# Performance work log

Measured on AMD Instinct MI355X. Metric: run time of the kernel, lower is better.

The kernel has to match this reference:

```python
import jax, jax.numpy as jnp
import numpy as np

D_MODEL = 2048
D_INNER = 4096
D_CONV = 4
D_STATE = 16
DT_RANK = 128  # (d_model + 15) // 16
EPS = 1e-5
B_SZ, SEQ = 2, 2048


def _silu(x):
    return x * jax.nn.sigmoid(x)


def setup_inputs() -> dict:
    key = jax.random.key(0)
    ks = jax.random.split(key, 10)
    s = lambda k, shape, sc=0.02: jax.random.normal(k, shape, jnp.float32) * sc
    # S4D-real init for A_log, small negative bias for dt (standard Mamba init)
    A_log = jnp.log(jnp.tile(jnp.arange(1, D_STATE + 1, dtype=jnp.float32), (D_INNER, 1)))
    return {
        "hidden_states": jax.random.normal(ks[0], (B_SZ, SEQ, D_MODEL), jnp.float32),
        "norm_scale": jnp.ones((D_MODEL,), jnp.float32),
        "in_proj_w": s(ks[1], (2 * D_INNER, D_MODEL)),
        "conv_w": s(ks[2], (D_INNER, 1, D_CONV), 0.1),
        "conv_b": s(ks[3], (D_INNER,), 0.1),
        "x_proj_w": s(ks[4], (DT_RANK + 2 * D_STATE, D_INNER)),
        "dt_proj_w": s(ks[5], (D_INNER, DT_RANK), 0.1),
        "dt_proj_b": jnp.full((D_INNER,), -4.0, jnp.float32) + s(ks[6], (D_INNER,), 0.1),
        "out_proj_w": s(ks[7], (D_MODEL, D_INNER)),
        "A_log": A_log,
        "D": jnp.ones((D_INNER,), jnp.float32),
    }


def reference(hidden_states, norm_scale, in_proj_w, conv_w, conv_b, x_proj_w,
              dt_proj_w, dt_proj_b, out_proj_w, A_log, D):
    B, L, _ = hidden_states.shape
    residual = hidden_states
    # RMSNorm
    rms = jnp.sqrt(jnp.mean(hidden_states ** 2, axis=-1, keepdims=True) + EPS)
    xn = hidden_states / rms * norm_scale
    # in_proj -> [B, L, 2*d_inner]; torch code keeps this as projected_states
    xz = jnp.einsum('bld,ed->ble', xn, in_proj_w)
    x_in = xz[..., :D_INNER].transpose(0, 2, 1)  # [B, d_inner, L]
    z = xz[..., D_INNER:]                        # [B, L, d_inner]
    # depthwise causal conv1d (padding d_conv-1, truncated to L) + SiLU
    xc = jax.lax.conv_general_dilated(
        x_in, conv_w, window_strides=(1,), padding=[(D_CONV - 1, 0)],
        feature_group_count=D_INNER)
    xc = _silu(xc + conv_b[None, :, None])       # [B, d_inner, L]
    # x_proj -> dt, B, C
    x_dbl = jnp.einsum('bdl,rd->brl', xc, x_proj_w)  # [B, dt_rank+2*d_state, L]
    dt_low = x_dbl[:, :DT_RANK]
    Bm = x_dbl[:, DT_RANK:DT_RANK + D_STATE]         # [B, d_state, L]
    Cm = x_dbl[:, DT_RANK + D_STATE:]                # [B, d_state, L]
    delta = jax.nn.softplus(
        jnp.einsum('dr,brl->bdl', dt_proj_w, dt_low) + dt_proj_b[None, :, None])
    A = -jnp.exp(A_log)                              # [d_inner, d_state]
    # selective scan: h_t = exp(delta_t * A) * h_{t-1} + delta_t * B_t * u_t
    delta_t = delta.transpose(2, 0, 1)  # [L, B, d_inner]
    u_t = xc.transpose(2, 0, 1)         # [L, B, d_inner]
    B_t = Bm.transpose(2, 0, 1)         # [L, B, d_state]
    C_t = Cm.transpose(2, 0, 1)         # [L, B, d_state]

    def step(h, inp):
        d_, b_, c_, u_ = inp
        dA = jnp.exp(d_[..., None] * A)                      # [B, d_inner, d_state]
        h = h * dA + (d_ * u_)[..., None] * b_[:, None, :]   # [B, d_inner, d_state]
        y = jnp.einsum('bds,bs->bd', h, c_)                  # [B, d_inner]
        return h, y

    h0 = jnp.zeros((B, D_INNER, D_STATE), hidden_states.dtype)
    _, ys = jax.lax.scan(step, h0, (delta_t, B_t, C_t, u_t))  # [L, B, d_inner]
    y = ys.transpose(1, 0, 2) + xc.transpose(0, 2, 1) * D     # [B, L, d_inner]
    y = y * _silu(z)
    out = jnp.einsum('bld,od->blo', y, out_proj_w)            # [B, L, d_model]
    return residual + out, xz
```

## Files before the change

kernel.cpp:

```cpp
#include <hip/hip_runtime.h>
#include <cstdint>
#include <cstddef>

#define DM   2048
#define DI   4096
#define DST  16
#define DTR  128
#define SEQL 2048
#define NTOK 4096
#define XZW  8192
#define NCHAIN 8192
#define CL   32
#define NCH  64

typedef short short8 __attribute__((ext_vector_type(8)));
typedef float f32x4 __attribute__((ext_vector_type(4)));

__device__ __forceinline__ short f2bf(float x) {
  union { float f; uint32_t u; } v; v.f = x;
  uint32_t r = v.u + 0x7fffu + ((v.u >> 16) & 1u);
  return (short)(r >> 16);
}
__device__ __forceinline__ float bf2f(short s) {
  union { uint32_t u; float f; } v; v.u = ((uint32_t)(uint16_t)s) << 16;
  return v.f;
}

__device__ __forceinline__ void stage16(const short* g, short* l) {
#if __has_builtin(__builtin_amdgcn_global_load_lds)
  __builtin_amdgcn_global_load_lds((const __attribute__((address_space(1))) void*)g,
                                   (__attribute__((address_space(3))) void*)l, 16, 0, 0);
#else
  *(short8*)l = *(const short8*)g;
#endif
}

__global__ __launch_bounds__(256) void cvt4_k(const float* __restrict__ in,
                                              short* __restrict__ out, int n4) {
  int i = blockIdx.x * 256 + threadIdx.x;
  if (i >= n4) return;
  float4 v = ((const float4*)in)[i];
  short4 o;
  o.x = f2bf(v.x); o.y = f2bf(v.y); o.z = f2bf(v.z); o.w = f2bf(v.w);
  ((short4*)out)[i] = o;
}

__global__ __launch_bounds__(256) void pad_xproj_k(const float* __restrict__ xp,
                                                   short* __restrict__ out) {
  int i = blockIdx.x * 256 + threadIdx.x;
  if (i >= 256 * 1024) return;
  int r = i >> 10;
  float4 v = make_float4(0.f, 0.f, 0.f, 0.f);
  if (r < 160) v = ((const float4*)xp)[i];
  short4 o;
  o.x = f2bf(v.x); o.y = f2bf(v.y); o.z = f2bf(v.z); o.w = f2bf(v.w);
  ((short4*)out)[i] = o;
}

__global__ __launch_bounds__(256) void rmsnorm_k(const float* __restrict__ hs,
                                                 const float* __restrict__ sc,
                                                 short* __restrict__ xn) {
  const int token = blockIdx.x;
  const int tid = threadIdx.x;
  const float* row = hs + (size_t)token * DM;
  float4 a = ((const float4*)row)[tid];
  float4 b = ((const float4*)row)[tid + 256];
  float ss = a.x*a.x + a.y*a.y + a.z*a.z + a.w*a.w
           + b.x*b.x + b.y*b.y + b.z*b.z + b.w*b.w;
  #pragma unroll
  for (int o = 32; o > 0; o >>= 1) ss += __shfl_xor(ss, o);
  __shared__ float wsum[4];
  if ((tid & 63) == 0) wsum[tid >> 6] = ss;
  __syncthreads();
  float tot = wsum[0] + wsum[1] + wsum[2] + wsum[3];
  float inv = rsqrtf(tot * (1.0f / DM) + 1e-5f);
  float4 s1 = ((const float4*)sc)[tid];
  float4 s2 = ((const float4*)sc)[tid + 256];
  short4 o1, o2;
  o1.x = f2bf(a.x * inv * s1.x); o1.y = f2bf(a.y * inv * s1.y);
  o1.z = f2bf(a.z * inv * s1.z); o1.w = f2bf(a.w * inv * s1.w);
  o2.x = f2bf(b.x * inv * s2.x); o2.y = f2bf(b.y * inv * s2.y);
  o2.z = f2bf(b.z * inv * s2.z); o2.w = f2bf(b.w * inv * s2.w);
  ((short4*)xn)[(size_t)token * (DM / 4) + tid] = o1;
  ((short4*)xn)[(size_t)token * (DM / 4) + tid + 256] = o2;
}

#define LGKM_FENCE() do { asm volatile("s_waitcnt lgkmcnt(0)" ::: "memory"); \
                          __builtin_amdgcn_sched_barrier(0); } while (0)

template <int MFR, int EPI, int RBY, int RBX, int PRE>
__global__ __launch_bounds__(512) void gemm_big(const short* __restrict__ A,
                                                const short* __restrict__ B,
                                                int K, int N, int nbx,
                                                float* __restrict__ out_f,
                                                const float* __restrict__ aux_f) {
  constexpr int BM = MFR * 32;
  constexpr int ABYTES = BM * 128;
  constexpr int BBYTES = 256 * 128;
  constexpr int AINSTR = ABYTES / 8192;
  constexpr int BUF = ABYTES + BBYTES;
  __shared__ char lds[2 * BUF];

  const int tid = threadIdx.x;
  const int lane = tid & 63;
  const int wid = tid >> 6;
  const int wm = wid >> 2;
  const int wn = wid & 3;
  const int lr = lane & 15;
  const int lj = lane >> 4;

  const int xcd = blockIdx.x & 7;
  const int idx = blockIdx.x >> 3;
  const int nrgx = nbx / RBX;
  const int by = (xcd / nrgx) * RBY + idx / RBX;
  const int bx = (xcd % nrgx) * RBX + idx % RBX;
  const size_t m0 = (size_t)by * BM;
  const size_t n0 = (size_t)bx * 256;

  const int NT = K >> 6;

  auto stA1 = [&](int t, char* buf, int s) {
    const int k0 = t << 6;
    const int off = s * 8192 + tid * 16;
    const int r = off >> 7;
    const int j = (off >> 4) & 7;
    stage16(A + (m0 + r) * (size_t)K + k0 + ((j ^ (r & 7)) << 3),
            (short*)(buf + off));
  };
  auto stB1 = [&](int t, char* buf, int s) {
    const int k0 = t << 6;
    const int off = s * 8192 + tid * 16;
    const int r = off >> 7;
    const int j = (off >> 4) & 7;
    stage16(B + (n0 + r) * (size_t)K + k0 + ((j ^ (r & 7)) << 3),
            (short*)(buf + ABYTES + off));
  };

#define READ_A(dst, fbase)                                                   \
  _Pragma("unroll")                                                          \
  for (int f = 0; f < MFR / 2; ++f) {                                        \
    const int arow = wm * (BM / 2) + ((fbase) + f) * 16 + lr;                \
    _Pragma("unroll")                                                        \
    for (int ks = 0; ks < 2; ++ks)                                           \
      dst[f][ks] = *(const short8*)(cur + arow * 128 +                       \
                     ((((ks << 2) + lj) ^ (arow & 7)) << 4));                \
  }
#define READ_B(dst, gbase)                                                   \
  _Pragma("unroll")                                                          \
  for (int g = 0; g < 2; ++g) {                                              \
    const int brow = wn * 64 + ((gbase) + g) * 16 + lr;                      \
    _Pragma("unroll")                                                        \
    for (int ks = 0; ks < 2; ++ks)                                           \
      dst[g][ks] = *(const short8*)(cur + ABYTES + brow * 128 +              \
                     ((((ks << 2) + lj) ^ (brow & 7)) << 4));                \
  }
#define MFMA_Q(fbase, gbase, bvx)                                            \
  __builtin_amdgcn_s_setprio(1);                                             \
  _Pragma("unroll")                                                          \
  for (int ks = 0; ks < 2; ++ks)                                             \
    _Pragma("unroll")                                                        \
    for (int f = 0; f < MFR / 2; ++f)                                        \
      _Pragma("unroll")                                                      \
      for (int g = 0; g < 2; ++g)                                            \
        acc[(fbase) + f][(gbase) + g] = __builtin_amdgcn_mfma_f32_16x16x32_bf16( \
            av[f][ks], bvx[g][ks], acc[(fbase) + f][(gbase) + g], 0, 0, 0);  \
  __builtin_amdgcn_s_setprio(0);

  f32x4 acc[MFR][4] = {};

  {
    #pragma unroll
    for (int s = 0; s < AINSTR; ++s) stA1(0, lds, s);
    #pragma unroll
    for (int s = 0; s < 4; ++s) stB1(0, lds, s);
    if (PRE && NT > 1) { stA1(1, lds + BUF, 0); stA1(1, lds + BUF, 2); }
    if (PRE && NT > 1) asm volatile("s_waitcnt vmcnt(2)" ::: "memory");
    else               asm volatile("s_waitcnt vmcnt(0)" ::: "memory");
    __builtin_amdgcn_s_barrier();
    __builtin_amdgcn_sched_barrier(0);
  }

  for (int t = 0; t < NT; ++t) {
    char* cur = lds + (t & 1) * BUF;
    char* nxt = lds + ((t + 1) & 1) * BUF;
    const bool m1 = (t + 1) < NT;
    const bool m2 = (t + 2) < NT;
    short8 av[MFR / 2][2], bv0[2][2], bv1[2][2];

    READ_A(av, 0);
    READ_B(bv0, 0);
    if (m1) {
      if constexpr (PRE) { stA1(t + 1, nxt, 1); stA1(t + 1, nxt, 3); }
      else {
        #pragma unroll
        for (int s = 0; s < AINSTR; ++s) stA1(t + 1, nxt, s);
      }
    }
    LGKM_FENCE();
    MFMA_Q(0, 0, bv0);
    __builtin_amdgcn_s_barrier();

    READ_B(bv1, 2);
    if (m1) { stB1(t + 1, nxt, 0); stB1(t + 1, nxt, 1); }
    LGKM_FENCE();
    MFMA_Q(0, 2, bv1);
    __builtin_amdgcn_s_barrier();

    READ_A(av, MFR / 2);
    if (m1) { stB1(t + 1, nxt, 2); stB1(t + 1, nxt, 3); }
    if (PRE && m2) { stA1(t + 2, cur, 0); stA1(t + 2, cur, 2); }
    LGKM_FENCE();
    MFMA_Q(MFR / 2, 2, bv1);
    __builtin_amdgcn_s_barrier();

    MFMA_Q(MFR / 2, 0, bv0);
    if (PRE && m2) asm volatile("s_waitcnt vmcnt(2)" ::: "memory");
    else           asm volatile("s_waitcnt vmcnt(0)" ::: "memory");
    __builtin_amdgcn_s_barrier();
    __builtin_amdgcn_sched_barrier(0);
  }

  #pragma unroll
  for (int f = 0; f < MFR; ++f)
    #pragma unroll
    for (int g = 0; g < 4; ++g)
      #pragma unroll
      for (int jj = 0; jj < 4; ++jj) {
        const size_t row = m0 + wm * (BM / 2) + f * 16 + lj * 4 + jj;
        const size_t col = n0 + wn * 64 + g * 16 + lr;
        float v = acc[f][g][jj];
        if constexpr (EPI == 3) v += aux_f[row * (size_t)N + col];
        out_f[row * (size_t)N + col] = v;
      }
#undef READ_A
#undef READ_B
#undef MFMA_Q
}

template <int EPI>
__global__ __launch_bounds__(256) void gemm_nt(const short* __restrict__ A,
                                               const short* __restrict__ B,
                                               int ld, int K, int N,
                                               float* __restrict__ out_f,
                                               const float* __restrict__ aux_f,
                                               short* __restrict__ out_bf) {
  __shared__ short As[128 * 64];
  __shared__ short Bs[128 * 64];
  const int tid = threadIdx.x;
  const int lane = tid & 63;
  const int wid = tid >> 6;
  const int wr = wid >> 1, wc = wid & 1;
  const size_t m0 = (size_t)blockIdx.y * 128;
  const size_t n0 = (size_t)blockIdx.x * 128;
  A += (size_t)blockIdx.z * K;
  B += (size_t)blockIdx.z * K;
  f32x4 acc[4][4] = {};
  for (int k0 = 0; k0 < K; k0 += 64) {
    #pragma unroll
    for (int i = 0; i < 4; ++i) {
      const int off = i * 4096 + tid * 16;
      const int r = off >> 7;
      const int ke = (off & 127) >> 1;
      stage16(A + (m0 + r) * (size_t)ld + k0 + ke, &As[off >> 1]);
      stage16(B + (n0 + r) * (size_t)ld + k0 + ke, &Bs[off >> 1]);
    }
    __syncthreads();
    #pragma unroll
    for (int kk = 0; kk < 64; kk += 32) {
      short8 af[4], bfr[4];
      const int kb = kk + (lane >> 4) * 8;
      const int rr = lane & 15;
      #pragma unroll
      for (int f = 0; f < 4; ++f) {
        af[f]  = *(const short8*)&As[(wr * 64 + f * 16 + rr) * 64 + kb];
        bfr[f] = *(const short8*)&Bs[(wc * 64 + f * 16 + rr) * 64 + kb];
      }
      #pragma unroll
      for (int fm = 0; fm < 4; ++fm)
        #pragma unroll
        for (int fn = 0; fn < 4; ++fn)
          acc[fm][fn] = __builtin_amdgcn_mfma_f32_16x16x32_bf16(af[fm], bfr[fn], acc[fm][fn], 0, 0, 0);
    }
    __syncthreads();
  }
  const int rbase = (lane >> 4) * 4;
  const int cbase = lane & 15;
  #pragma unroll
  for (int fm = 0; fm < 4; ++fm) {
    #pragma unroll
    for (int fn = 0; fn < 4; ++fn) {
      #pragma unroll
      for (int j = 0; j < 4; ++j) {
        const size_t row = m0 + wr * 64 + fm * 16 + rbase + j;
        const size_t col = n0 + wc * 64 + fn * 16 + cbase;
        const float v = acc[fm][fn][j];
        if constexpr (EPI == 2) {
          float x = v + aux_f[col];
          float sp = (x > 20.f) ? x : log1pf(__expf(x));
          out_bf[row * (size_t)N + col] = f2bf(sp);
        } else {
          out_f[((size_t)blockIdx.z * NTOK + row) * (size_t)N + col] = v;
        }
      }
    }
  }
}

__global__ __launch_bounds__(256) void xdbl_epi_k(const float* __restrict__ part,
                                                  short* __restrict__ dtl,
                                                  float* __restrict__ Bc,
                                                  float* __restrict__ Cc) {
  const int row = blockIdx.x;
  const int col = threadIdx.x;
  const size_t i = (size_t)row * 256 + col;
  const float v = part[i] + part[(size_t)NTOK * 256 + i]
                + part[(size_t)2 * NTOK * 256 + i]
                + part[(size_t)3 * NTOK * 256 + i];
  if (col < 128)      dtl[(size_t)row * 128 + col] = f2bf(v);
  else if (col < 144) Bc[(size_t)row * 16 + (col - 128)] = v;
  else if (col < 160) Cc[(size_t)row * 16 + (col - 144)] = v;
}

__global__ __launch_bounds__(256) void conv_silu_k(const float* __restrict__ xz,
                                                   const float* __restrict__ cw,
                                                   const float* __restrict__ cb,
                                                   short* __restrict__ xc) {
  const int d = blockIdx.x * 256 + threadIdx.x;
  const int t0 = blockIdx.y * 8;
  const int l0 = t0 & (SEQL - 1);
  const float4 w = ((const float4*)cw)[d];
  const float bias = cb[d];
  float x0 = (l0 >= 3) ? xz[(size_t)(t0 - 3) * XZW + d] : 0.f;
  float x1 = (l0 >= 2) ? xz[(size_t)(t0 - 2) * XZW + d] : 0.f;
  float x2 = (l0 >= 1) ? xz[(size_t)(t0 - 1) * XZW + d] : 0.f;
  #pragma unroll
  for (int i = 0; i < 8; ++i) {
    const float x3 = xz[(size_t)(t0 + i) * XZW + d];
    const float acc = bias + w.x * x0 + w.y * x1 + w.z * x2 + w.w * x3;
    const float sv = acc / (1.f + __expf(-acc));
    xc[(size_t)(t0 + i) * DI + d] = f2bf(sv);
    x0 = x1; x1 = x2; x2 = x3;
  }
}

__global__ __launch_bounds__(256) void scan1_k(const short* __restrict__ del_bf,
                                               const short* __restrict__ xc,
                                               const float* __restrict__ Bc,
                                               const float* __restrict__ alog,
                                               float* __restrict__ hloc,
                                               float* __restrict__ Ssum) {
  const int t = blockIdx.x * 256 + threadIdx.x;
  const int sub = t & 1;
  const int chain = (t >> 1) & (NCHAIN - 1);
  const int chunk = t >> 14;
  const int b = chain >> 12;
  const int d = chain & 4095;
  float A[8];
  #pragma unroll
  for (int j = 0; j < 8; ++j) A[j] = -__expf(alog[d * 16 + sub * 8 + j]);
  float h[8] = {};
  float S = 0.f;
  size_t token = (size_t)b * SEQL + (size_t)chunk * CL;
  #pragma unroll 2
  for (int l = 0; l < CL; ++l, ++token) {
    const float delta = bf2f(del_bf[token * DI + d]);
    const float u = bf2f(xc[token * DI + d]);
    const float du = delta * u;
    S += delta;
    const float4 B0 = ((const float4*)Bc)[token * 4 + sub * 2];
    const float4 B1 = ((const float4*)Bc)[token * 4 + sub * 2 + 1];
    const float Bv[8] = {B0.x, B0.y, B0.z, B0.w, B1.x, B1.y, B1.z, B1.w};
    #pragma unroll
    for (int j = 0; j < 8; ++j)
      h[j] = h[j] * __expf(delta * A[j]) + du * Bv[j];
  }
  const size_t idx = (size_t)(chunk * NCHAIN + chain) * 4 + sub * 2;
  ((float4*)hloc)[idx]     = make_float4(h[0], h[1], h[2], h[3]);
  ((float4*)hloc)[idx + 1] = make_float4(h[4], h[5], h[6], h[7]);
  if (sub == 0) Ssum[chunk * NCHAIN + chain] = S;
}

__global__ __launch_bounds__(256) void scan2_k(float* __restrict__ hloc,
                                               const float* __restrict__ Ssum,
                                               const float* __restrict__ alog) {
  const int t = blockIdx.x * 256 + threadIdx.x;
  const int q = t & 3;
  const int chain = t >> 2;
  const int d = chain & 4095;
  float A[4];
  #pragma unroll
  for (int j = 0; j < 4; ++j) A[j] = -__expf(alog[d * 16 + q * 4 + j]);
  float4 h = make_float4(0.f, 0.f, 0.f, 0.f);
  for (int c = 0; c < NCH; ++c) {
    const size_t idx = (size_t)(c * NCHAIN + chain) * 4 + q;
    const float S = Ssum[c * NCHAIN + chain];
    const float4 hl = ((const float4*)hloc)[idx];
    ((float4*)hloc)[idx] = h;
    h.x = h.x * __expf(A[0] * S) + hl.x;
    h.y = h.y * __expf(A[1] * S) + hl.y;
    h.z = h.z * __expf(A[2] * S) + hl.z;
    h.w = h.w * __expf(A[3] * S) + hl.w;
  }
}

__global__ __launch_bounds__(256) void scan3_k(const short* __restrict__ del_bf,
                                               const short* __restrict__ xc,
                                               const float* __restrict__ Bc,
                                               const float* __restrict__ Cc,
                                               const float* __restrict__ xzbuf,
                                               const float* __restrict__ alog,
                                               const float* __restrict__ dvec,
                                               const float* __restrict__ hin,
                                               short* __restrict__ y) {
  const int t = blockIdx.x * 256 + threadIdx.x;
  const int sub = t & 1;
  const int chain = (t >> 1) & (NCHAIN - 1);
  const int chunk = t >> 14;
  const int b = chain >> 12;
  const int d = chain & 4095;
  float A[8];
  #pragma unroll
  for (int j = 0; j < 8; ++j) A[j] = -__expf(alog[d * 16 + sub * 8 + j]);
  const float Dd = dvec[d];
  const size_t idx = (size_t)(chunk * NCHAIN + chain) * 4 + sub * 2;
  const float4 h0 = ((const float4*)hin)[idx];
  const float4 h1 = ((const float4*)hin)[idx + 1];
  float h[8] = {h0.x, h0.y, h0.z, h0.w, h1.x, h1.y, h1.z, h1.w};
  size_t token = (size_t)b * SEQL + (size_t)chunk * CL;
  #pragma unroll 2
  for (int l = 0; l < CL; ++l, ++token) {
    const float delta = bf2f(del_bf[token * DI + d]);
    const float u = bf2f(xc[token * DI + d]);
    const float du = delta * u;
    const float4 B0 = ((const float4*)Bc)[token * 4 + sub * 2];
    const float4 B1 = ((const float4*)Bc)[token * 4 + sub * 2 + 1];
    const float4 C0 = ((const float4*)Cc)[token * 4 + sub * 2];
    const float4 C1 = ((const float4*)Cc)[token * 4 + sub * 2 + 1];
    const float Bv[8] = {B0.x, B0.y, B0.z, B0.w, B1.x, B1.y, B1.z, B1.w};
    const float Cv[8] = {C0.x, C0.y, C0.z, C0.w, C1.x, C1.y, C1.z, C1.w};
    float yp = 0.f;
    #pragma unroll
    for (int j = 0; j < 8; ++j) {
      h[j] = h[j] * __expf(delta * A[j]) + du * Bv[j];
      yp += h[j] * Cv[j];
    }
    yp += __shfl_xor(yp, 1);
    if (sub == 0) {
      const float z = xzbuf[token * XZW + DI + d];
      const float sz = z / (1.f + __expf(-z));
      y[token * DI + d] = f2bf((yp + u * Dd) * sz);
    }
  }
}

extern "C" void kernel_launch(void* const* d_in, const int* in_sizes, int n_in,
                              void* d_out, int out_size, void* d_ws, size_t ws_size,
                              hipStream_t stream) {
  const float* hs   = (const float*)d_in[0];
  const float* nsc  = (const float*)d_in[1];
  const float* win  = (const float*)d_in[2];
  const float* cw   = (const float*)d_in[3];
  const float* cb   = (const float*)d_in[4];
  const float* wxp  = (const float*)d_in[5];
  const float* wdt  = (const float*)d_in[6];
  const float* bdt  = (const float*)d_in[7];
  const float* wout = (const float*)d_in[8];
  const float* alog = (const float*)d_in[9];
  const float* dvec = (const float*)d_in[10];

  float* out0 = (float*)d_out;
  float* xz   = out0 + (size_t)NTOK * DM;

  char* w = (char*)d_ws;
  size_t off = 0;
  auto alloc = [&](size_t bytes) {
    char* p = w + off;
    off += (bytes + 255) & ~(size_t)255;
    return p;
  };
  short* xn_bf   = (short*)alloc((size_t)NTOK * DM * 2);
  short* win_bf  = (short*)alloc((size_t)XZW * DM * 2);
  short* wout_bf = (short*)alloc((size_t)DM * DI * 2);
  short* wdt_bf  = (short*)alloc((size_t)DI * DTR * 2);
  short* wxp_bf  = (short*)alloc((size_t)256 * DI * 2);
  short* xc_bf   = (short*)alloc((size_t)NTOK * DI * 2);
  short* dtl_bf  = (short*)alloc((size_t)NTOK * DTR * 2);
  float* Bc      = (float*)alloc((size_t)NTOK * DST * 4);
  float* Cc      = (float*)alloc((size_t)NTOK * DST * 4);
  short* del_bf  = (short*)alloc((size_t)NTOK * DI * 2);
  short* y_bf    = (short*)alloc((size_t)NTOK * DI * 2);

  float* xp_part = (float*)win_bf;
  float* hloc    = (float*)win_bf;
  float* Ssum    = (float*)xn_bf;

  cvt4_k<<<16384, 256, 0, stream>>>(win,  win_bf,  (XZW * DM) / 4);
  cvt4_k<<<8192,  256, 0, stream>>>(wout, wout_bf, (DM * DI) / 4);
  cvt4_k<<<512,   256, 0, stream>>>(wdt,  wdt_bf,  (DI * DTR) / 4);
  pad_xproj_k<<<1024, 256, 0, stream>>>(wxp, wxp_bf);

  rmsnorm_k<<<NTOK, 256, 0, stream>>>(hs, nsc, xn_bf);
  gemm_big<8, 0, 8, 8, 1><<<dim3((XZW / 256) * (NTOK / 256)), 512, 0, stream>>>(
      xn_bf, win_bf, DM, XZW, XZW / 256, xz, nullptr);
  conv_silu_k<<<dim3(DI / 256, NTOK / 8), 256, 0, stream>>>(xz, cw, cb, xc_bf);
  gemm_nt<4><<<dim3(2, NTOK / 128, 4), 256, 0, stream>>>(
      xc_bf, wxp_bf, DI, DI / 4, 256, xp_part, nullptr, nullptr);
  xdbl_epi_k<<<NTOK, 256, 0, stream>>>(xp_part, dtl_bf, Bc, Cc);
  gemm_nt<2><<<dim3(DI / 128, NTOK / 128, 1), 256, 0, stream>>>(
      dtl_bf, wdt_bf, DTR, DTR, DI, nullptr, bdt, del_bf);
  scan1_k<<<(NCHAIN * 2 * NCH) / 256, 256, 0, stream>>>(
      del_bf, xc_bf, Bc, alog, hloc, Ssum);
  scan2_k<<<(NCHAIN * 4) / 256, 256, 0, stream>>>(hloc, Ssum, alog);
  scan3_k<<<(NCHAIN * 2 * NCH) / 256, 256, 0, stream>>>(
      del_bf, xc_bf, Bc, Cc, xz, alog, dvec, hloc, y_bf);
  gemm_big<4, 3, 8, 4, 0><<<dim3((DM / 256) * (NTOK / 128)), 512, 0, stream>>>(
      y_bf, wout_bf, DI, DM, DM / 256, out0, hs);
}
```

Baseline: 570.7 us.

## Stage B tiles through registers in big GEMM and skip padded x_proj columns

The big GEMM no longer prefetches A two tiles ahead. B tiles for the next step are now loaded from global memory into registers early in each iteration and written to LDS at the end, replacing the direct global-to-LDS staging of B. This is meant to hide B load latency behind the MFMA work, at the cost of more registers and an extra LDS write phase. Separately, the x_proj GEMM epilogue and the reduction kernel skip the padded columns at or beyond 160, saving wasted stores and reads.

Measured after the change: 573.6 us. Within noise of the previous version (+0.5%).

```diff
diff --git a/kernel.cpp b/kernel.cpp
--- a/kernel.cpp
+++ b/kernel.cpp
@@ -88,7 +88,7 @@
 #define LGKM_FENCE() do { asm volatile("s_waitcnt lgkmcnt(0)" ::: "memory"); \
                           __builtin_amdgcn_sched_barrier(0); } while (0)
 
-template <int MFR, int EPI, int RBY, int RBX, int PRE>
+template <int MFR, int EPI, int RBY, int RBX>
 __global__ __launch_bounds__(512) void gemm_big(const short* __restrict__ A,
                                                 const short* __restrict__ B,
                                                 int K, int N, int nbx,
@@ -135,6 +135,13 @@
     stage16(B + (n0 + r) * (size_t)K + k0 + ((j ^ (r & 7)) << 3),
             (short*)(buf + ABYTES + off));
   };
+  auto bsrc = [&](int t, int s) -> const int4* {
+    const int k0 = t << 6;
+    const int off = s * 8192 + tid * 16;
+    const int r = off >> 7;
+    const int j = (off >> 4) & 7;
+    return (const int4*)(B + (n0 + r) * (size_t)K + k0 + ((j ^ (r & 7)) << 3));
+  };
 
 #define READ_A(dst, fbase)                                                   \
   _Pragma("unroll")                                                          \
@@ -173,9 +180,7 @@
     for (int s = 0; s < AINSTR; ++s) stA1(0, lds, s);
     #pragma unroll
     for (int s = 0; s < 4; ++s) stB1(0, lds, s);
-    if (PRE && NT > 1) { stA1(1, lds + BUF, 0); stA1(1, lds + BUF, 2); }
-    if (PRE && NT > 1) asm volatile("s_waitcnt vmcnt(2)" ::: "memory");
-    else               asm volatile("s_waitcnt vmcnt(0)" ::: "memory");
+    asm volatile("s_waitcnt vmcnt(0)" ::: "memory");
     __builtin_amdgcn_s_barrier();
     __builtin_amdgcn_sched_barrier(0);
   }
@@ -184,38 +189,43 @@
     char* cur = lds + (t & 1) * BUF;
     char* nxt = lds + ((t + 1) & 1) * BUF;
     const bool m1 = (t + 1) < NT;
-    const bool m2 = (t + 2) < NT;
     short8 av[MFR / 2][2], bv0[2][2], bv1[2][2];
+    int4 breg0, breg1, breg2, breg3;
 
     READ_A(av, 0);
     READ_B(bv0, 0);
     if (m1) {
-      if constexpr (PRE) { stA1(t + 1, nxt, 1); stA1(t + 1, nxt, 3); }
-      else {
-        #pragma unroll
-        for (int s = 0; s < AINSTR; ++s) stA1(t + 1, nxt, s);
-      }
+      #pragma unroll
+      for (int s = 0; s < AINSTR; ++s) stA1(t + 1, nxt, s);
+      breg0 = *bsrc(t + 1, 0);
+      breg1 = *bsrc(t + 1, 1);
+      breg2 = *bsrc(t + 1, 2);
+      breg3 = *bsrc(t + 1, 3);
     }
     LGKM_FENCE();
     MFMA_Q(0, 0, bv0);
     __builtin_amdgcn_s_barrier();
 
     READ_B(bv1, 2);
-    if (m1) { stB1(t + 1, nxt, 0); stB1(t + 1, nxt, 1); }
     LGKM_FENCE();
     MFMA_Q(0, 2, bv1);
     __builtin_amdgcn_s_barrier();
 
     READ_A(av, MFR / 2);
-    if (m1) { stB1(t + 1, nxt, 2); stB1(t + 1, nxt, 3); }
-    if (PRE && m2) { stA1(t + 2, cur, 0); stA1(t + 2, cur, 2); }
     LGKM_FENCE();
     MFMA_Q(MFR / 2, 2, bv1);
     __builtin_amdgcn_s_barrier();
 
     MFMA_Q(MFR / 2, 0, bv0);
-    if (PRE && m2) asm volatile("s_waitcnt vmcnt(2)" ::: "memory");
-    else           asm volatile("s_waitcnt vmcnt(0)" ::: "memory");
+    if (m1) {
+      *(int4*)(nxt + ABYTES + 0 * 8192 + tid * 16) = breg0;
+      *(int4*)(nxt + ABYTES + 1 * 8192 + tid * 16) = breg1;
+      *(int4*)(nxt + ABYTES + 2 * 8192 + tid * 16) = breg2;
+      *(int4*)(nxt + ABYTES + 3 * 8192 + tid * 16) = breg3;
+    } else {
+      asm volatile("s_waitcnt vmcnt(0)" ::: "memory");
+    }
+    LGKM_FENCE();
     __builtin_amdgcn_s_barrier();
     __builtin_amdgcn_sched_barrier(0);
   }
@@ -299,7 +309,8 @@
           float sp = (x > 20.f) ? x : log1pf(__expf(x));
           out_bf[row * (size_t)N + col] = f2bf(sp);
         } else {
-          out_f[((size_t)blockIdx.z * NTOK + row) * (size_t)N + col] = v;
+          if (col < 160)
+            out_f[((size_t)blockIdx.z * NTOK + row) * (size_t)N + col] = v;
         }
       }
     }
@@ -312,13 +323,14 @@
                                                   float* __restrict__ Cc) {
   const int row = blockIdx.x;
   const int col = threadIdx.x;
+  if (col >= 160) return;
   const size_t i = (size_t)row * 256 + col;
   const float v = part[i] + part[(size_t)NTOK * 256 + i]
                 + part[(size_t)2 * NTOK * 256 + i]
                 + part[(size_t)3 * NTOK * 256 + i];
   if (col < 128)      dtl[(size_t)row * 128 + col] = f2bf(v);
   else if (col < 144) Bc[(size_t)row * 16 + (col - 128)] = v;
-  else if (col < 160) Cc[(size_t)row * 16 + (col - 144)] = v;
+  else                Cc[(size_t)row * 16 + (col - 144)] = v;
 }
 
 __global__ __launch_bounds__(256) void conv_silu_k(const float* __restrict__ xz,
@@ -500,7 +512,7 @@
   pad_xproj_k<<<1024, 256, 0, stream>>>(wxp, wxp_bf);
 
   rmsnorm_k<<<NTOK, 256, 0, stream>>>(hs, nsc, xn_bf);
-  gemm_big<8, 0, 8, 8, 1><<<dim3((XZW / 256) * (NTOK / 256)), 512, 0, stream>>>(
+  gemm_big<8, 0, 8, 8><<<dim3((XZW / 256) * (NTOK / 256)), 512, 0, stream>>>(
       xn_bf, win_bf, DM, XZW, XZW / 256, xz, nullptr);
   conv_silu_k<<<dim3(DI / 256, NTOK / 8), 256, 0, stream>>>(xz, cw, cb, xc_bf);
   gemm_nt<4><<<dim3(2, NTOK / 128, 4), 256, 0, stream>>>(
@@ -513,6 +525,6 @@
   scan2_k<<<(NCHAIN * 4) / 256, 256, 0, stream>>>(hloc, Ssum, alog);
   scan3_k<<<(NCHAIN * 2 * NCH) / 256, 256, 0, stream>>>(
       del_bf, xc_bf, Bc, Cc, xz, alog, dvec, hloc, y_bf);
-  gemm_big<4, 3, 8, 4, 0><<<dim3((DM / 256) * (NTOK / 128)), 512, 0, stream>>>(
+  gemm_big<4, 3, 8, 4><<<dim3((DM / 256) * (NTOK / 128)), 512, 0, stream>>>(
       y_bf, wout_bf, DI, DM, DM / 256, out0, hs);
 }
```
